# Kernel optimization log

Measured on AMD Instinct MI355X. Metric: run time of the kernel, lower is better.

Reference implementation:

```python
import jax, jax.numpy as jnp
import numpy as np

N = 50000
E = 1600000
F_IN = 128
F_OUT = 64
NEG_SLOPE = 0.2


def setup_inputs() -> dict:
    key = jax.random.key(0)
    k1, k2, k3, k4, k5, k6 = jax.random.split(key, 6)
    x = jax.random.normal(k1, (N, F_IN), dtype=jnp.float32)
    edge_index = jax.random.randint(k2, (2, E), 0, N, dtype=jnp.int64)
    # GATConv params (heads=1): glorot-ish scale
    W = jax.random.normal(k3, (F_IN, F_OUT), dtype=jnp.float32) * (1.0 / np.sqrt(F_IN))
    att_src = jax.random.normal(k4, (F_OUT,), dtype=jnp.float32) * (1.0 / np.sqrt(F_OUT))
    att_dst = jax.random.normal(k5, (F_OUT,), dtype=jnp.float32) * (1.0 / np.sqrt(F_OUT))
    bias = jnp.zeros((F_OUT,), dtype=jnp.float32)
    return {"x": x, "edge_index": edge_index, "W": W, "att_src": att_src, "att_dst": att_dst, "bias": bias}


def _gat_forward(x, edge_index, W, att_src, att_dst, bias):
    n = x.shape[0]
    # add self loops (PyG GATConv default)
    loops = jnp.arange(n, dtype=edge_index.dtype)
    src = jnp.concatenate([edge_index[0], loops])  # [E+N]
    dst = jnp.concatenate([edge_index[1], loops])  # [E+N]

    h = x @ W                                      # [N, F_OUT]
    a_src = h @ att_src                            # [N]
    a_dst = h @ att_dst                            # [N]

    e = a_src[src] + a_dst[dst]                    # [E+N]
    e = jnp.where(e > 0, e, NEG_SLOPE * e)         # LeakyReLU(0.2)

    # softmax over edges grouped by destination node
    e_max = jax.ops.segment_max(e, dst, num_segments=n)     # [N]
    e_exp = jnp.exp(e - e_max[dst])                          # [E+N]
    e_sum = jax.ops.segment_sum(e_exp, dst, num_segments=n)  # [N]
    alpha = e_exp / e_sum[dst]                               # [E+N]

    msg = h[src] * alpha[:, None]                            # [E+N, F_OUT]
    out = jax.ops.segment_sum(msg, dst, num_segments=n)      # [N, F_OUT]
    out = out + bias
    return jax.nn.relu(out)


def reference(x, edge_index, W, att_src, att_dst, bias):
    return _gat_forward(x, edge_index, W, att_src, att_dst, bias)
```

## Files before the change

### kernel.cpp

```cpp
#include <hip/hip_runtime.h>

#define NN 50000
#define NE 1600000
#define FIN 128
#define FOUT 64
#define SLOPE 0.2f

#define NPB  16
#define NBF  3125
#define CAPB 768
#define FBLK 261
#define CHC4 1536
#define GBLK 782
#define LW   136

typedef unsigned int u32;
typedef short short8 __attribute__((ext_vector_type(8)));
typedef float f32x4 __attribute__((ext_vector_type(4)));

__device__ __forceinline__ unsigned short f2bf(float f) {
    u32 u = __float_as_uint(f);
    u += 0x7FFFu + ((u >> 16) & 1u);
    return (unsigned short)(u >> 16);
}
__device__ __forceinline__ float bf2f(unsigned short s) {
    return __uint_as_float(((u32)s) << 16);
}

union FusedLds {
    unsigned short Wt[64 * LW];
    struct { int cnt[NBF]; int gb[NBF]; } f;
};

__global__ __launch_bounds__(256) void fused_k(
        const float* __restrict__ x, const float* __restrict__ W,
        const float* __restrict__ att_s, const float* __restrict__ att_d,
        const int* __restrict__ ei, int* __restrict__ fcur,
        u32* __restrict__ fstage, unsigned short* __restrict__ h,
        float* __restrict__ a_src, float* __restrict__ a_dst) {
    __shared__ FusedLds L;
    const int tid = threadIdx.x;

    if (blockIdx.x < FBLK) {
        for (int i = tid; i < NBF; i += 256) L.f.cnt[i] = 0;
        __syncthreads();
        const int4* sd4 = (const int4*)(ei + NE);
        const int4* ss4 = (const int4*)ei;
        const int lo = blockIdx.x * CHC4, hi = min(NE / 4, lo + CHC4);
        for (int i = lo + tid; i < hi; i += 256) {
            int4 d = sd4[i];
            atomicAdd(&L.f.cnt[d.x >> 4], 1);
            atomicAdd(&L.f.cnt[d.y >> 4], 1);
            atomicAdd(&L.f.cnt[d.z >> 4], 1);
            atomicAdd(&L.f.cnt[d.w >> 4], 1);
        }
        __syncthreads();
        for (int b = tid; b < NBF; b += 256) {
            int tot = L.f.cnt[b];
            L.f.gb[b] = tot ? atomicAdd(&fcur[b], tot) : 0;
            L.f.cnt[b] = 0;
        }
        __syncthreads();
        for (int i = lo + tid; i < hi; i += 256) {
            int4 d = sd4[i];
            int4 s = ss4[i];
            int b, pos;
            b = d.x >> 4; pos = L.f.gb[b] + atomicAdd(&L.f.cnt[b], 1);
            if (pos < CAPB) fstage[(size_t)b * CAPB + pos] = (u32)s.x | ((u32)(d.x & 15) << 16);
            b = d.y >> 4; pos = L.f.gb[b] + atomicAdd(&L.f.cnt[b], 1);
            if (pos < CAPB) fstage[(size_t)b * CAPB + pos] = (u32)s.y | ((u32)(d.y & 15) << 16);
            b = d.z >> 4; pos = L.f.gb[b] + atomicAdd(&L.f.cnt[b], 1);
            if (pos < CAPB) fstage[(size_t)b * CAPB + pos] = (u32)s.z | ((u32)(d.z & 15) << 16);
            b = d.w >> 4; pos = L.f.gb[b] + atomicAdd(&L.f.cnt[b], 1);
            if (pos < CAPB) fstage[(size_t)b * CAPB + pos] = (u32)s.w | ((u32)(d.w & 15) << 16);
        }
    } else {
        unsigned short* Wt = L.Wt;
        const int node0 = (blockIdx.x - FBLK) * 64;
        for (int i = tid; i < 128 * 16; i += 256) {
            int k = i >> 4, f = (i & 15) * 4;
            float4 w4 = ((const float4*)W)[i];
            Wt[(f + 0) * LW + k] = f2bf(w4.x);
            Wt[(f + 1) * LW + k] = f2bf(w4.y);
            Wt[(f + 2) * LW + k] = f2bf(w4.z);
            Wt[(f + 3) * LW + k] = f2bf(w4.w);
        }
        const int wv = tid >> 6, lane = tid & 63;
        const int q = lane >> 4, mr = lane & 15;
        const int row = node0 + wv * 16 + mr;
        const bool valid = row < NN;
        const float4* x4 = (const float4*)x;

        short8 afr[4];
        #pragma unroll
        for (int ks = 0; ks < 4; ++ks) {
            float4 f0 = make_float4(0.f, 0.f, 0.f, 0.f), f1 = f0;
            if (valid) {
                f0 = x4[(size_t)row * 32 + ks * 8 + q * 2];
                f1 = x4[(size_t)row * 32 + ks * 8 + q * 2 + 1];
            }
            short8 a;
            a[0] = (short)f2bf(f0.x); a[1] = (short)f2bf(f0.y);
            a[2] = (short)f2bf(f0.z); a[3] = (short)f2bf(f0.w);
            a[4] = (short)f2bf(f1.x); a[5] = (short)f2bf(f1.y);
            a[6] = (short)f2bf(f1.z); a[7] = (short)f2bf(f1.w);
            afr[ks] = a;
        }
        __syncthreads();

        f32x4 acc[4] = {{0,0,0,0},{0,0,0,0},{0,0,0,0},{0,0,0,0}};
        #pragma unroll
        for (int ks = 0; ks < 4; ++ks) {
            #pragma unroll
            for (int nt = 0; nt < 4; ++nt) {
                short8 b = *(const short8*)(Wt + (nt * 16 + mr) * LW + ks * 32 + q * 8);
                acc[nt] = __builtin_amdgcn_mfma_f32_16x16x32_bf16(afr[ks], b, acc[nt], 0, 0, 0);
            }
        }
        float atts[4], attd[4];
        #pragma unroll
        for (int nt = 0; nt < 4; ++nt) {
            atts[nt] = att_s[nt * 16 + mr];
            attd[nt] = att_d[nt * 16 + mr];
        }
        #pragma unroll
        for (int r = 0; r < 4; ++r) {
            int node = node0 + wv * 16 + q * 4 + r;
            float ps = 0.f, pd = 0.f;
            #pragma unroll
            for (int nt = 0; nt < 4; ++nt) {
                float v = acc[nt][r];
                if (node < NN) h[(size_t)node * 64 + nt * 16 + mr] = f2bf(v);
                ps += v * atts[nt];
                pd += v * attd[nt];
            }
            #pragma unroll
            for (int off = 8; off > 0; off >>= 1) {
                ps += __shfl_xor(ps, off);
                pd += __shfl_xor(pd, off);
            }
            if (mr == 0 && node < NN) { a_src[node] = ps; a_dst[node] = pd; }
        }
    }
}

__global__ __launch_bounds__(256) void agg_k(
        const u32* __restrict__ staging, const int* __restrict__ bcur,
        const float* __restrict__ a_src, const float* __restrict__ a_dst,
        const ushort4* __restrict__ h4, const float* __restrict__ bias,
        float* __restrict__ out) {
    const int bkt = blockIdx.x;
    const int node0 = bkt << 4;
    const int nNodes = min(NPB, NN - node0);
    const int bsize = min(bcur[bkt], CAPB);
    const u32* stg = staging + (size_t)bkt * CAPB;
    const int tid = threadIdx.x, wv = tid >> 6, lane = tid & 63;

    __shared__ u32 pk[CAPB];
    __shared__ unsigned short ssrc[CAPB];
    __shared__ int lcnt[NPB];
    __shared__ int lbase[NPB + 1];
    __shared__ int lcur[NPB];
    float* evals = (float*)pk;

    for (int j = tid; j < bsize; j += 256) pk[j] = stg[j];
    if (tid < NPB) lcnt[tid] = 0;
    __syncthreads();
    for (int j = tid; j < bsize; j += 256)
        atomicAdd(&lcnt[pk[j] >> 16], 1);
    __syncthreads();
    if (tid < 64) {
        int v = (tid < NPB) ? lcnt[tid] : 0;
        #pragma unroll
        for (int off = 1; off < NPB; off <<= 1) {
            int u = __shfl_up(v, off);
            if (tid >= off) v += u;
        }
        if (tid < NPB) lbase[tid + 1] = v;
        if (tid == 0) lbase[0] = 0;
    }
    if (tid >= 64 && tid < 64 + NPB) lcur[tid - 64] = 0;
    __syncthreads();
    for (int j = tid; j < bsize; j += 256) {
        u32 w = pk[j];
        int ld = w >> 16;
        int pos = lbase[ld] + atomicAdd(&lcur[ld], 1);
        ssrc[pos] = (unsigned short)(w & 0xFFFFu);
    }
    __syncthreads();

    const int q = lane >> 4, ql = lane & 15;
    const float4 b4 = ((const float4*)bias)[ql];
    const int ln = wv * 4 + q;
    if (ln >= nNodes) return;
    const int n = node0 + ln;
    const int st = lbase[ln], deg = lbase[ln + 1] - st;
    const float ad = a_dst[n];
    float es = a_src[n] + ad; es = es > 0.f ? es : SLOPE * es;
    const float ps = __expf(es);
    float sum = 0.f;
    for (int j = ql; j < deg; j += 16) {
        int s = ssrc[st + j];
        float e = a_src[s] + ad; e = e > 0.f ? e : SLOPE * e;
        float pe = __expf(e);
        evals[st + j] = pe;
        sum += pe;
    }
    sum += __shfl_xor(sum, 8); sum += __shfl_xor(sum, 4);
    sum += __shfl_xor(sum, 2); sum += __shfl_xor(sum, 1);
    const float inv = 1.f / (sum + ps);

    ushort4 hs = h4[(size_t)n * 16 + ql];
    float a0 = ps * bf2f(hs.x), a1 = ps * bf2f(hs.y);
    float a2 = ps * bf2f(hs.z), a3 = ps * bf2f(hs.w);
    int j = 0;
    for (; j + 4 <= deg; j += 4) {
        int s0 = ssrc[st + j], s1 = ssrc[st + j + 1];
        int s2 = ssrc[st + j + 2], s3 = ssrc[st + j + 3];
        float e0 = evals[st + j], e1 = evals[st + j + 1];
        float e2 = evals[st + j + 2], e3 = evals[st + j + 3];
        ushort4 v0 = h4[(size_t)s0 * 16 + ql];
        ushort4 v1 = h4[(size_t)s1 * 16 + ql];
        ushort4 v2 = h4[(size_t)s2 * 16 + ql];
        ushort4 v3 = h4[(size_t)s3 * 16 + ql];
        a0 += e0 * bf2f(v0.x); a1 += e0 * bf2f(v0.y);
        a2 += e0 * bf2f(v0.z); a3 += e0 * bf2f(v0.w);
        a0 += e1 * bf2f(v1.x); a1 += e1 * bf2f(v1.y);
        a2 += e1 * bf2f(v1.z); a3 += e1 * bf2f(v1.w);
        a0 += e2 * bf2f(v2.x); a1 += e2 * bf2f(v2.y);
        a2 += e2 * bf2f(v2.z); a3 += e2 * bf2f(v2.w);
        a0 += e3 * bf2f(v3.x); a1 += e3 * bf2f(v3.y);
        a2 += e3 * bf2f(v3.z); a3 += e3 * bf2f(v3.w);
    }
    for (; j < deg; ++j) {
        int s = ssrc[st + j];
        float ev = evals[st + j];
        ushort4 hv = h4[(size_t)s * 16 + ql];
        a0 += ev * bf2f(hv.x); a1 += ev * bf2f(hv.y);
        a2 += ev * bf2f(hv.z); a3 += ev * bf2f(hv.w);
    }
    float4 o;
    o.x = a0 * inv + b4.x; o.x = o.x > 0.f ? o.x : 0.f;
    o.y = a1 * inv + b4.y; o.y = o.y > 0.f ? o.y : 0.f;
    o.z = a2 * inv + b4.z; o.z = o.z > 0.f ? o.z : 0.f;
    o.w = a3 * inv + b4.w; o.w = o.w > 0.f ? o.w : 0.f;
    ((float4*)out)[(size_t)n * 16 + ql] = o;
}

extern "C" void kernel_launch(void* const* d_in, const int* in_sizes, int n_in,
                              void* d_out, int out_size, void* d_ws, size_t ws_size,
                              hipStream_t stream) {
    const float* x     = (const float*)d_in[0];
    const int*   ei    = (const int*)d_in[1];
    const float* W     = (const float*)d_in[2];
    const float* att_s = (const float*)d_in[3];
    const float* att_d = (const float*)d_in[4];
    const float* bias  = (const float*)d_in[5];
    float* out = (float*)d_out;

    unsigned short* h = (unsigned short*)d_ws;
    float* a_src  = (float*)(h + (size_t)NN * 64);
    float* a_dst  = a_src + NN;
    int*   fcur   = (int*)(a_dst + NN);
    u32*   fstage = (u32*)(fcur + 3200);

    hipMemsetAsync(fcur, 0, NBF * sizeof(int), stream);

    fused_k<<<FBLK + GBLK, 256, 0, stream>>>(x, W, att_s, att_d, ei, fcur,
                                             fstage, h, a_src, a_dst);
    agg_k<<<NBF, 256, 0, stream>>>(fstage, fcur, a_src, a_dst,
                                   (const ushort4*)h, bias, out);
}
```

Baseline: 146.6 us.

## Run GEMM and edge bucketing in every block, holding edges in registers

Previously the fused kernel split its blocks into two roles: some bucketed edges by destination and the rest computed the bf16 projection. Now every one of the 782 blocks first does its GEMM tile and then buckets a 512-int4 slice of edges (CHC4 drops from 1536 to 512, so 782×512 covers the 400000 int4s). Bucket ids and packed payloads are kept in registers between the count pass and the scatter pass, so the edge list is read from global memory once instead of twice. The aim is to balance work across blocks and cut edge-index traffic. The cost is more register pressure and one extra LDS reset and barriers per block, and the GEMM and bucketing phases in a block now run one after the other instead of overlapping across blocks.

New measurement: 169.2 us. 1.15x slower.

```diff
diff --git a/kernel.cpp b/kernel.cpp
--- a/kernel.cpp
+++ b/kernel.cpp
@@ -2,6 +2,7 @@
 
 #define NN 50000
 #define NE 1600000
+#define NE4 400000
 #define FIN 128
 #define FOUT 64
 #define SLOPE 0.2f
@@ -9,9 +10,8 @@
 #define NPB  16
 #define NBF  3125
 #define CAPB 768
-#define FBLK 261
-#define CHC4 1536
 #define GBLK 782
+#define CHC4 512
 #define LW   136
 
 typedef unsigned int u32;
@@ -41,42 +41,9 @@
     __shared__ FusedLds L;
     const int tid = threadIdx.x;
 
-    if (blockIdx.x < FBLK) {
-        for (int i = tid; i < NBF; i += 256) L.f.cnt[i] = 0;
-        __syncthreads();
-        const int4* sd4 = (const int4*)(ei + NE);
-        const int4* ss4 = (const int4*)ei;
-        const int lo = blockIdx.x * CHC4, hi = min(NE / 4, lo + CHC4);
-        for (int i = lo + tid; i < hi; i += 256) {
-            int4 d = sd4[i];
-            atomicAdd(&L.f.cnt[d.x >> 4], 1);
-            atomicAdd(&L.f.cnt[d.y >> 4], 1);
-            atomicAdd(&L.f.cnt[d.z >> 4], 1);
-            atomicAdd(&L.f.cnt[d.w >> 4], 1);
-        }
-        __syncthreads();
-        for (int b = tid; b < NBF; b += 256) {
-            int tot = L.f.cnt[b];
-            L.f.gb[b] = tot ? atomicAdd(&fcur[b], tot) : 0;
-            L.f.cnt[b] = 0;
-        }
-        __syncthreads();
-        for (int i = lo + tid; i < hi; i += 256) {
-            int4 d = sd4[i];
-            int4 s = ss4[i];
-            int b, pos;
-            b = d.x >> 4; pos = L.f.gb[b] + atomicAdd(&L.f.cnt[b], 1);
-            if (pos < CAPB) fstage[(size_t)b * CAPB + pos] = (u32)s.x | ((u32)(d.x & 15) << 16);
-            b = d.y >> 4; pos = L.f.gb[b] + atomicAdd(&L.f.cnt[b], 1);
-            if (pos < CAPB) fstage[(size_t)b * CAPB + pos] = (u32)s.y | ((u32)(d.y & 15) << 16);
-            b = d.z >> 4; pos = L.f.gb[b] + atomicAdd(&L.f.cnt[b], 1);
-            if (pos < CAPB) fstage[(size_t)b * CAPB + pos] = (u32)s.z | ((u32)(d.z & 15) << 16);
-            b = d.w >> 4; pos = L.f.gb[b] + atomicAdd(&L.f.cnt[b], 1);
-            if (pos < CAPB) fstage[(size_t)b * CAPB + pos] = (u32)s.w | ((u32)(d.w & 15) << 16);
-        }
-    } else {
+    {
         unsigned short* Wt = L.Wt;
-        const int node0 = (blockIdx.x - FBLK) * 64;
+        const int node0 = blockIdx.x * 64;
         for (int i = tid; i < 128 * 16; i += 256) {
             int k = i >> 4, f = (i & 15) * 4;
             float4 w4 = ((const float4*)W)[i];
@@ -140,6 +107,52 @@
                 pd += __shfl_xor(pd, off);
             }
             if (mr == 0 && node < NN) { a_src[node] = ps; a_dst[node] = pd; }
+        }
+    }
+    __syncthreads();
+
+    for (int i = tid; i < NBF; i += 256) L.f.cnt[i] = 0;
+    __syncthreads();
+
+    const int4* sd4 = (const int4*)(ei + NE);
+    const int4* ss4 = (const int4*)ei;
+    const int lo = blockIdx.x * CHC4;
+    int bkx[2][4];
+    u32 payx[2][4];
+    #pragma unroll
+    for (int u = 0; u < 2; ++u) {
+        const int i = lo + tid + u * 256;
+        if (i < NE4) {
+            int4 d = sd4[i];
+            int4 s = ss4[i];
+            bkx[u][0] = d.x >> 4; payx[u][0] = (u32)s.x | ((u32)(d.x & 15) << 16);
+            bkx[u][1] = d.y >> 4; payx[u][1] = (u32)s.y | ((u32)(d.y & 15) << 16);
+            bkx[u][2] = d.z >> 4; payx[u][2] = (u32)s.z | ((u32)(d.z & 15) << 16);
+            bkx[u][3] = d.w >> 4; payx[u][3] = (u32)s.w | ((u32)(d.w & 15) << 16);
+            atomicAdd(&L.f.cnt[bkx[u][0]], 1);
+            atomicAdd(&L.f.cnt[bkx[u][1]], 1);
+            atomicAdd(&L.f.cnt[bkx[u][2]], 1);
+            atomicAdd(&L.f.cnt[bkx[u][3]], 1);
+        } else {
+            bkx[u][0] = bkx[u][1] = bkx[u][2] = bkx[u][3] = -1;
+        }
+    }
+    __syncthreads();
+    for (int b = tid; b < NBF; b += 256) {
+        int tot = L.f.cnt[b];
+        L.f.gb[b] = tot ? atomicAdd(&fcur[b], tot) : 0;
+        L.f.cnt[b] = 0;
+    }
+    __syncthreads();
+    #pragma unroll
+    for (int u = 0; u < 2; ++u) {
+        #pragma unroll
+        for (int e = 0; e < 4; ++e) {
+            int b = bkx[u][e];
+            if (b >= 0) {
+                int pos = L.f.gb[b] + atomicAdd(&L.f.cnt[b], 1);
+                if (pos < CAPB) fstage[(size_t)b * CAPB + pos] = payx[u][e];
+            }
         }
     }
 }
@@ -266,8 +279,8 @@
 
     hipMemsetAsync(fcur, 0, NBF * sizeof(int), stream);
 
-    fused_k<<<FBLK + GBLK, 256, 0, stream>>>(x, W, att_s, att_d, ei, fcur,
-                                             fstage, h, a_src, a_dst);
+    fused_k<<<GBLK, 256, 0, stream>>>(x, W, att_s, att_d, ei, fcur,
+                                      fstage, h, a_src, a_dst);
     agg_k<<<NBF, 256, 0, stream>>>(fstage, fcur, a_src, a_dst,
                                    (const ushort4*)h, bias, out);
 }
```
